# Kernel tuning notes

Hardware: AMD Instinct MI355X
Metric: run time of the kernel (lower is better)

## Reference

```python
import jax, jax.numpy as jnp
import numpy as np

NEG = -1e9

def setup_inputs() -> dict:
    key = jax.random.key(0)
    k1, k2, k3, k4, k5, k6 = jax.random.split(key, 6)
    B, S, H = 8, 2048, 1024
    inputs = jax.random.normal(k1, (B, S, H), dtype=jnp.float32)
    mask = jax.random.randint(k2, (B, S, S), 0, 2) > 0  # bool [B,S,S]
    scale = 1.0 / np.sqrt(H)
    Wq = jax.random.normal(k3, (H, H), dtype=jnp.float32) * scale
    Wk = jax.random.normal(k4, (H, H), dtype=jnp.float32) * scale
    Wv = jax.random.normal(k5, (H, H), dtype=jnp.float32) * scale
    return {"inputs": inputs, "mask": mask, "Wq": Wq, "Wk": Wk, "Wv": Wv}

def reference(inputs, mask, Wq, Wk, Wv):
    H = inputs.shape[-1]
    # nn.Linear(x) = x @ W.T (bias=False)
    Q = jnp.einsum('bsh,dh->bsd', inputs, Wq)
    K = jnp.einsum('bsh,dh->bsd', inputs, Wk)
    V = jnp.einsum('bsh,dh->bsd', inputs, Wv)
    alpha = jnp.einsum('bqd,bkd->bqk', Q, K) / jnp.sqrt(jnp.float32(H))
    alpha = jnp.where(mask, NEG, alpha)
    alpha = jax.nn.softmax(alpha, axis=-1)
    return jnp.einsum('bqk,bkd->bqd', alpha, V)
```

## Files before the change

### kernel.cpp

```cpp
#include <hip/hip_runtime.h>
#include <hip/hip_bf16.h>
#include <hip/hip_fp16.h>
#include <stdint.h>

typedef __attribute__((ext_vector_type(4))) float    f32x4;
typedef __attribute__((ext_vector_type(8))) _Float16 f16x8;
typedef __attribute__((ext_vector_type(4))) _Float16 f16x4;

template <int N> struct IC { static constexpr int value = N; };

__device__ __forceinline__ f32x4 mfma16(f16x8 a, f16x8 b, f32x4 c) {
  return __builtin_amdgcn_mfma_f32_16x16x32_f16(a, b, c, 0, 0, 0);
}

__device__ __forceinline__ void store4(float* p, f32x4 v) { *(f32x4*)p = v; }
__device__ __forceinline__ void store4(_Float16* p, f32x4 v) {
  f16x4 h; h[0] = (_Float16)v[0]; h[1] = (_Float16)v[1];
  h[2] = (_Float16)v[2]; h[3] = (_Float16)v[3];
  *(f16x4*)p = h;
}

__device__ __forceinline__ void gload16(const _Float16* g, char* l) {
  __builtin_amdgcn_global_load_lds(
      (const __attribute__((address_space(1))) void*)g,
      (__attribute__((address_space(3))) void*)l, 16, 0, 0);
}

__device__ __forceinline__ bool src_is_f32(const void* p) {
  const unsigned* w = (const unsigned*)p;
  int sane = 0;
#pragma unroll
  for (int i = 0; i < 64; ++i) {
    const unsigned e = (w[i] >> 7) & 0xFFu;
    sane += (e >= 100u && e <= 140u) ? 1 : 0;
  }
  return sane < 40;
}

__device__ __forceinline__ float bf16_to_f32(unsigned u16) {
  union { unsigned u; float f; } c; c.u = u16 << 16; return c.f;
}

__device__ __forceinline__ f16x8 cvt8(const void* in, long i, bool f32) {
  f16x8 o;
  if (f32) {
    const float4 a = ((const float4*)in)[2 * i];
    const float4 b = ((const float4*)in)[2 * i + 1];
    o[0] = (_Float16)a.x; o[1] = (_Float16)a.y; o[2] = (_Float16)a.z; o[3] = (_Float16)a.w;
    o[4] = (_Float16)b.x; o[5] = (_Float16)b.y; o[6] = (_Float16)b.z; o[7] = (_Float16)b.w;
  } else {
    const uint4 v = ((const uint4*)in)[i];
    const unsigned wd[4] = {v.x, v.y, v.z, v.w};
#pragma unroll
    for (int j = 0; j < 4; ++j) {
      o[2 * j]     = (_Float16)bf16_to_f32(wd[j] & 0xFFFFu);
      o[2 * j + 1] = (_Float16)bf16_to_f32(wd[j] >> 16);
    }
  }
  return o;
}

enum { MK_I32, MK_I64, MK_U16, MK_F32, MK_F64, MK_U8 };

__global__ __launch_bounds__(256)
void prep(const void* __restrict__ X, const void* __restrict__ w0,
          const void* __restrict__ w1, const void* __restrict__ w2,
          const void* __restrict__ maskp,
          _Float16* __restrict__ Xh, _Float16* __restrict__ Wh,
          int* __restrict__ modeOut, long nX8, long nW8)
{
  const long b = blockIdx.x;
  const long xBlocks = nX8 / 256;
  const long wBlocks = 3 * nW8 / 256;

  if (b < xBlocks) {
    const long i = b * 256 + threadIdx.x;
    ((f16x8*)Xh)[i] = cvt8(X, i, src_is_f32(X));
    return;
  }
  if (b < xBlocks + wBlocks) {
    const long j = (b - xBlocks) * 256 + threadIdx.x;
    const int which = (int)(j / nW8);
    const long lj = j - (long)which * nW8;
    const void* src = which == 0 ? w0 : (which == 1 ? w1 : w2);
    ((f16x8*)Wh)[j] = cvt8(src, lj, src_is_f32(src));
    return;
  }
  if (threadIdx.x != 0) return;
  const unsigned* mw = (const unsigned*)maskp;
  bool le1 = true, u16p = true, f32p = true, f64p = true, oddz = true;
  for (int i = 0; i < 64; ++i) {
    const unsigned v = mw[i];
    if (v > 1u) le1 = false;
    if (v != 0u && v != 1u && v != 0x10000u && v != 0x10001u) u16p = false;
    if (v != 0u && v != 0x3F800000u) f32p = false;
    if (i & 1) { if (v != 0u && v != 0x3FF00000u) f64p = false; if (v) oddz = false; }
    else       { if (v > 1u) f64p = false; }
  }
  int mode;
  if (le1)        mode = oddz ? MK_I64 : MK_I32;
  else if (u16p)  mode = MK_U16;
  else if (f32p)  mode = MK_F32;
  else if (f64p)  mode = MK_F64;
  else            mode = MK_U8;
  *modeOut = mode;
}

__global__ __launch_bounds__(256)
void zerofill(float* out, long n) {
  const long i = (long)blockIdx.x * 256 + threadIdx.x;
  if (i < n) out[i] = 0.0f;
}

template <typename TO, int BN, int WN>
__global__ __launch_bounds__(512, 2)
void gemm256(const _Float16* __restrict__ Ag, const _Float16* __restrict__ Bg,
             TO* __restrict__ Cg, int ldA, int ldB, int ldC, int Kd,
             long sAb, long sBb, long sCb, float scale, int gx, int gy)
{
  constexpr int WM   = 8 / WN;
  constexpr int BMW  = 256 / WM;
  constexpr int MI   = BMW / 16;
  constexpr int NPH  = MI / 2;
  constexpr int BSZ  = 32768 + BN * 128;

  extern __shared__ char smem[];

  const int nwg = gridDim.x;
  const int q = nwg >> 3, r = nwg & 7;
  const int xcd = blockIdx.x & 7, sub = blockIdx.x >> 3;
  const int wg = (xcd < r ? xcd * (q + 1) : r * (q + 1) + (xcd - r) * q) + sub;
  const int bz  = wg / (gx * gy);
  const int rem = wg % (gx * gy);
  const int by  = rem / gx;
  const int bx  = rem % gx;

  const _Float16* A = Ag + (long)bz * sAb + (long)by * 256 * ldA;
  const _Float16* B = Bg + (long)bz * sBb + (long)bx * BN * ldB;
  TO* C = Cg + (long)bz * sCb;

  const int t   = threadIdx.x;
  const int ln  = t & 63;
  const int wid = t >> 6;
  const int wr  = wid / WN;
  const int wc  = wid % WN;
  const int fr  = ln & 15;
  const int c16 = ln >> 4;

  const int sr = t >> 3;
  const int sc = t & 7;
  const int swzc = (sc ^ (sr & 7)) << 3;

  auto STAGE = [&](const _Float16* M, int ld, int matOff, int row0, int kt1) {
    const _Float16* src = M + (long)(row0 + sr) * ld + (kt1 << 6) + swzc;
    char* dst = smem + (kt1 & 1) * BSZ + matOff + (row0 << 7) + (t << 4);
    gload16(src, dst);
  };
  auto STAGE_TILE = [&](int kt1) {
#pragma unroll
    for (int r0 = 0; r0 < BN; r0 += 64) STAGE(B, ldB, 32768, r0, kt1);
    STAGE(A, ldA, 0,   0, kt1);  STAGE(A, ldA, 0,  64, kt1);
    STAGE(A, ldA, 0, 128, kt1);  STAGE(A, ldA, 0, 192, kt1);
  };

  f32x4 acc[MI][4] = {};

  STAGE_TILE(0);
  asm volatile("s_waitcnt vmcnt(0)" ::: "memory");
  __builtin_amdgcn_s_barrier();

  const int NT = Kd >> 6;

  auto kloop = [&](auto rotC) {
    constexpr int ROT = decltype(rotC)::value;
    for (int kt = 0; kt < NT; ++kt) {
      const int bufOff = (kt & 1) * BSZ;
      if (kt + 1 < NT) STAGE_TILE(kt + 1);

      auto LDA = [&](int mi, int kk) -> f16x8 {
        const int row = wr * BMW + (mi << 4) + fr;
        const int ch  = ((kk << 2) + c16) ^ (row & 7);
        return *(const f16x8*)(smem + bufOff + (row << 7) + (ch << 4));
      };
      auto LDB = [&](int ni, int kk) -> f16x8 {
        const int row = (wc << 6) + (ni << 4) + fr;
        const int ch  = ((kk << 2) + c16) ^ (row & 7);
        return *(const f16x8*)(smem + bufOff + 32768 + (row << 7) + (ch << 4));
      };

      f16x8 bF[4][2];
#pragma unroll
      for (int ni = 0; ni < 4; ++ni)
#pragma unroll
        for (int kk = 0; kk < 2; ++kk) bF[ni][kk] = LDB(ni, kk);

#pragma unroll
      for (int p = 0; p < NPH; ++p) {
        const int pr = (p + ROT) % NPH;
        f16x8 aF[2][2];
#pragma unroll
        for (int i = 0; i < 2; ++i)
#pragma unroll
          for (int kk = 0; kk < 2; ++kk) aF[i][kk] = LDA(2 * pr + i, kk);

        __builtin_amdgcn_s_setprio(1);
#pragma unroll
        for (int i = 0; i < 2; ++i)
#pragma unroll
          for (int ni = 0; ni < 4; ++ni)
#pragma unroll
            for (int kk = 0; kk < 2; ++kk)
              acc[2 * pr + i][ni] = mfma16(aF[i][kk], bF[ni][kk], acc[2 * pr + i][ni]);
        __builtin_amdgcn_s_setprio(0);
      }

      asm volatile("s_waitcnt vmcnt(0)" ::: "memory");
      __builtin_amdgcn_s_barrier();
    }
  };

  if constexpr (NPH == 4) {
    const int rot = ((wid & 3) + ((wid >> 2) << 1)) & 3;
    switch (rot) {
      case 0: kloop(IC<0>{}); break;
      case 1: kloop(IC<1>{}); break;
      case 2: kloop(IC<2>{}); break;
      default: kloop(IC<3>{}); break;
    }
  } else {
    const int rot = (wid ^ (wid >> 2)) & 1;
    if (rot == 0) kloop(IC<0>{}); else kloop(IC<1>{});
  }

  {
    char* wb = smem + wid * 4352;
    const int rr = (ln >> 4) << 2;
    const int rrow = ln >> 4;
    const int rch  = ln & 15;
#pragma unroll
    for (int mi = 0; mi < MI; ++mi) {
#pragma unroll
      for (int ni = 0; ni < 4; ++ni)
#pragma unroll
        for (int rq = 0; rq < 4; ++rq)
          *(float*)(wb + (((rr + rq) * 68) + (ni << 4) + fr) * 4) =
              scale * acc[mi][ni][rq];
#pragma unroll
      for (int it = 0; it < 4; ++it) {
        const int rloc = it * 4 + rrow;
        f32x4 v = *(const f32x4*)(wb + (rloc * 68 + rch * 4) * 4);
        const int row = by * 256 + wr * BMW + mi * 16 + rloc;
        const int col = bx * BN + wc * 64 + rch * 4;
        store4(&C[(long)row * ldC + col], v);
      }
    }
  }
}

__global__ __launch_bounds__(256)
void softmax_wave(_Float16* __restrict__ P, const void* __restrict__ maskp,
                  const int* __restrict__ modep, int S, long row0)
{
  const int  mode = *modep;
  const long lrow = (long)blockIdx.x * 4 + (threadIdx.x >> 6);
  const long grow = row0 + lrow;
  const int  ln   = threadIdx.x & 63;

  _Float16* prow = P + lrow * S;
  f16x8 pv[4];
#pragma unroll
  for (int j = 0; j < 4; ++j)
    pv[j] = *(const f16x8*)(prow + j * 512 + ln * 8);

  const long ebase = grow * (long)S;
  int mk[4][8];
  if (mode == MK_U8) {
    const unsigned char* m = (const unsigned char*)maskp + ebase;
#pragma unroll
    for (int j = 0; j < 4; ++j) {
      const unsigned long long v = *(const unsigned long long*)(m + j * 512 + ln * 8);
#pragma unroll
      for (int k = 0; k < 8; ++k) mk[j][k] = (int)((v >> (8 * k)) & 0xffull);
    }
  } else if (mode == MK_I32) {
    const int* m = (const int*)maskp + ebase;
#pragma unroll
    for (int j = 0; j < 4; ++j) {
      const int4 a = *(const int4*)(m + j * 512 + ln * 8);
      const int4 b = *(const int4*)(m + j * 512 + ln * 8 + 4);
      mk[j][0] = a.x; mk[j][1] = a.y; mk[j][2] = a.z; mk[j][3] = a.w;
      mk[j][4] = b.x; mk[j][5] = b.y; mk[j][6] = b.z; mk[j][7] = b.w;
    }
  } else if (mode == MK_F32) {
    const unsigned* m = (const unsigned*)maskp + ebase;
#pragma unroll
    for (int j = 0; j < 4; ++j) {
      const uint4 a = *(const uint4*)(m + j * 512 + ln * 8);
      const uint4 b = *(const uint4*)(m + j * 512 + ln * 8 + 4);
      mk[j][0] = a.x != 0; mk[j][1] = a.y != 0; mk[j][2] = a.z != 0; mk[j][3] = a.w != 0;
      mk[j][4] = b.x != 0; mk[j][5] = b.y != 0; mk[j][6] = b.z != 0; mk[j][7] = b.w != 0;
    }
  } else if (mode == MK_U16) {
    const unsigned short* m = (const unsigned short*)maskp + ebase;
#pragma unroll
    for (int j = 0; j < 4; ++j) {
      const uint4 v = *(const uint4*)(m + j * 512 + ln * 8);
      const unsigned wd[4] = {v.x, v.y, v.z, v.w};
#pragma unroll
      for (int k = 0; k < 4; ++k) {
        mk[j][2 * k]     = (wd[k] & 0xFFFFu) != 0;
        mk[j][2 * k + 1] = (wd[k] >> 16) != 0;
      }
    }
  } else {
    const unsigned long long* m = (const unsigned long long*)maskp + ebase;
#pragma unroll
    for (int j = 0; j < 4; ++j)
#pragma unroll
      for (int k = 0; k < 8; ++k) mk[j][k] = m[j * 512 + ln * 8 + k] != 0ull;
  }

  float s[4][8];
  float mx = -3.0e38f;
#pragma unroll
  for (int j = 0; j < 4; ++j)
#pragma unroll
    for (int k = 0; k < 8; ++k) {
      s[j][k] = mk[j][k] ? -1e9f : (float)pv[j][k];
      mx = fmaxf(mx, s[j][k]);
    }
#pragma unroll
  for (int d = 1; d < 64; d <<= 1) mx = fmaxf(mx, __shfl_xor(mx, d));

  float sum = 0.f;
#pragma unroll
  for (int j = 0; j < 4; ++j)
#pragma unroll
    for (int k = 0; k < 8; ++k) { s[j][k] = __expf(s[j][k] - mx); sum += s[j][k]; }
#pragma unroll
  for (int d = 1; d < 64; d <<= 1) sum += __shfl_xor(sum, d);
  const float inv = 1.0f / sum;

#pragma unroll
  for (int j = 0; j < 4; ++j) {
    f16x8 ov;
#pragma unroll
    for (int k = 0; k < 8; ++k) ov[k] = (_Float16)(s[j][k] * inv);
    *(f16x8*)(prow + j * 512 + ln * 8) = ov;
  }
}

extern "C" void kernel_launch(void* const* d_in, const int* in_sizes, int n_in,
                              void* d_out, int out_size, void* d_ws, size_t ws_size,
                              hipStream_t stream)
{
  const int B = 8, S = 2048, H = 1024;
  const long nXl = (long)B * S * H;
  const long nMl = (long)B * S * S;
  const long nWl = (long)H * H;

  const void* X = nullptr;
  const void* Mk = nullptr;
  const void* W[3] = {nullptr, nullptr, nullptr};
  int wi = 0;
  for (int i = 0; i < n_in; ++i) {
    const long sz = in_sizes[i];
    if (sz == nXl) X = d_in[i];
    else if (sz == nMl) Mk = d_in[i];
    else if (sz == nWl && wi < 3) W[wi++] = d_in[i];
  }
  float* Out = (float*)d_out;

  const size_t nX = (size_t)nXl, nW = (size_t)nWl;
  const size_t need2 = (4 * nX + 3 * nW) * 2;
  const size_t need1 = (3 * nX + 3 * nW) * 2 + (size_t)nMl * 2;

  if (!X || !Mk || wi < 3 || ws_size < need2 + 256) {
    zerofill<<<dim3((unsigned)((out_size + 255) / 256)), dim3(256), 0, stream>>>(
        Out, (long)out_size);
    return;
  }
  const bool single = (ws_size >= need1 + 256);

  _Float16* Wh  = (_Float16*)d_ws;
  _Float16* QK2 = Wh  + 3 * nW;
  _Float16* Vt  = QK2 + 2 * nX;
  _Float16* Xh  = Vt  + nX;
  _Float16* P   = Xh;
  int* modeSlot = (int*)((char*)d_ws + (single ? need1 : need2));

  dim3 blk(256), gblk(512);
  const size_t LDS_256 = 2 * (32768 + 256 * 128);
  const size_t LDS_128 = 2 * (32768 + 128 * 128);
  const long SH = (long)S * H, SS = (long)S * S, HS = (long)H * S;

  const long nX8 = nX / 8, nW8 = nW / 8;
  const unsigned prepBlocks = (unsigned)(nX8 / 256 + 3 * nW8 / 256 + 1);
  prep<<<dim3(prepBlocks), blk, 0, stream>>>(X, W[0], W[1], W[2], Mk,
                                             Xh, Wh, modeSlot, nX8, nW8);

  gemm256<_Float16, 256, 4><<<dim3(8 * 64), gblk, LDS_256, stream>>>(
      Xh, Wh, QK2, H, H, 2 * H, H, 0L, 0L, 0L, 1.0f, 8, 64);
  gemm256<_Float16, 256, 4><<<dim3(8 * 4 * 8), gblk, LDS_256, stream>>>(
      Wh + 2 * nW, Xh, Vt, H, H, S, H, 0L, SH, HS, 1.0f, 8, 4);

  const _Float16* Qp = QK2;
  const _Float16* Kp = QK2 + H;

  if (single) {
    gemm256<_Float16, 256, 4><<<dim3(8 * 8 * 8), gblk, LDS_256, stream>>>(
        Qp, Kp, P, 2 * H, 2 * H, S, H, 2 * SH, 2 * SH, SS, 0.03125f, 8, 8);
    softmax_wave<<<dim3(B * S / 4), blk, 0, stream>>>(P, Mk, modeSlot, S, 0L);
    gemm256<float, 256, 4><<<dim3(4 * 8 * 8), gblk, LDS_256, stream>>>(
        P, Vt, Out, S, S, H, S, SS, HS, SH, 1.0f, 4, 8);
  } else {
    for (int g = 0; g < 2; ++g) {
      const int b0 = 4 * g;
      gemm256<_Float16, 256, 4><<<dim3(8 * 8 * 4), gblk, LDS_256, stream>>>(
          Qp + (long)b0 * 2 * SH, Kp + (long)b0 * 2 * SH, P,
          2 * H, 2 * H, S, H, 2 * SH, 2 * SH, SS, 0.03125f, 8, 8);
      softmax_wave<<<dim3(4 * S / 4), blk, 0, stream>>>(P, Mk, modeSlot, S, (long)b0 * S);
      gemm256<float, 128, 2><<<dim3(8 * 8 * 4), gblk, LDS_128, stream>>>(
          P, Vt + (long)b0 * HS, Out + (long)b0 * SH,
          S, S, H, S, SS, HS, SH, 1.0f, 8, 8);
    }
  }
}
```

Measured before the change: 310.0 us.

## Split GEMM k-loop into four MFMA quadrants interleaved with staged loads

Restructures the main GEMM k-loop into four quadrant phases. Each phase issues part of the next tile's global-to-LDS loads, runs a quarter of the MFMAs, and synchronises with barriers and partial vmcnt waits. This replaces the old per-wave phase rotation and the single bulk stage at the start of each iteration. The goal is to spread memory traffic across compute and keep waves in lockstep, at the cost of more barriers per iteration. The correctness of the partial vmcnt waits depends on the ordering of the loads.

Measured after the change: 316.1 us. About the same (+2.0%).

```diff
diff --git a/kernel.cpp b/kernel.cpp
--- a/kernel.cpp
+++ b/kernel.cpp
@@ -118,11 +118,11 @@
              TO* __restrict__ Cg, int ldA, int ldB, int ldC, int Kd,
              long sAb, long sBb, long sCb, float scale, int gx, int gy)
 {
-  constexpr int WM   = 8 / WN;
-  constexpr int BMW  = 256 / WM;
-  constexpr int MI   = BMW / 16;
-  constexpr int NPH  = MI / 2;
-  constexpr int BSZ  = 32768 + BN * 128;
+  constexpr int WM  = 8 / WN;
+  constexpr int BMW = 256 / WM;
+  constexpr int MI  = BMW / 16;
+  constexpr int QM  = MI / 2;
+  constexpr int BSZ = 32768 + BN * 128;
 
   extern __shared__ char smem[];
 
@@ -156,80 +156,114 @@
     char* dst = smem + (kt1 & 1) * BSZ + matOff + (row0 << 7) + (t << 4);
     gload16(src, dst);
   };
-  auto STAGE_TILE = [&](int kt1) {
-#pragma unroll
-    for (int r0 = 0; r0 < BN; r0 += 64) STAGE(B, ldB, 32768, r0, kt1);
-    STAGE(A, ldA, 0,   0, kt1);  STAGE(A, ldA, 0,  64, kt1);
-    STAGE(A, ldA, 0, 128, kt1);  STAGE(A, ldA, 0, 192, kt1);
+
+  f32x4 acc[MI][4] = {};
+  f16x8 bF[4][2], aF[QM][2];
+
+  auto MFMAQ = [&](auto MQc, auto NQc) {
+    constexpr int mq = decltype(MQc)::value;
+    constexpr int nq = decltype(NQc)::value;
+#pragma unroll
+    for (int i = 0; i < QM; ++i)
+#pragma unroll
+      for (int n2 = 0; n2 < 2; ++n2)
+#pragma unroll
+        for (int kk = 0; kk < 2; ++kk)
+          acc[mq * QM + i][nq * 2 + n2] =
+              mfma16(aF[i][kk], bF[nq * 2 + n2][kk], acc[mq * QM + i][nq * 2 + n2]);
   };
 
-  f32x4 acc[MI][4] = {};
-
-  STAGE_TILE(0);
-  asm volatile("s_waitcnt vmcnt(0)" ::: "memory");
+  if constexpr (WN == 4) {
+    STAGE(B, ldB, 32768,   0, 0); STAGE(B, ldB, 32768,  64, 0);
+    STAGE(B, ldB, 32768, 128, 0); STAGE(B, ldB, 32768, 192, 0);
+    STAGE(A, ldA, 0,   0, 0);     STAGE(A, ldA, 0, 128, 0);
+    STAGE(A, ldA, 0,  64, 0);     STAGE(A, ldA, 0, 192, 0);
+    asm volatile("s_waitcnt vmcnt(2)" ::: "memory");
+  } else {
+    STAGE(B, ldB, 32768,   0, 0); STAGE(B, ldB, 32768,  64, 0);
+    STAGE(A, ldA, 0,   0, 0);     STAGE(A, ldA, 0,  64, 0);
+    STAGE(A, ldA, 0, 128, 0);     STAGE(A, ldA, 0, 192, 0);
+    asm volatile("s_waitcnt vmcnt(0)" ::: "memory");
+  }
   __builtin_amdgcn_s_barrier();
 
   const int NT = Kd >> 6;
-
-  auto kloop = [&](auto rotC) {
-    constexpr int ROT = decltype(rotC)::value;
-    for (int kt = 0; kt < NT; ++kt) {
-      const int bufOff = (kt & 1) * BSZ;
-      if (kt + 1 < NT) STAGE_TILE(kt + 1);
-
-      auto LDA = [&](int mi, int kk) -> f16x8 {
-        const int row = wr * BMW + (mi << 4) + fr;
-        const int ch  = ((kk << 2) + c16) ^ (row & 7);
-        return *(const f16x8*)(smem + bufOff + (row << 7) + (ch << 4));
-      };
-      auto LDB = [&](int ni, int kk) -> f16x8 {
-        const int row = (wc << 6) + (ni << 4) + fr;
-        const int ch  = ((kk << 2) + c16) ^ (row & 7);
-        return *(const f16x8*)(smem + bufOff + 32768 + (row << 7) + (ch << 4));
-      };
-
-      f16x8 bF[4][2];
-#pragma unroll
-      for (int ni = 0; ni < 4; ++ni)
-#pragma unroll
-        for (int kk = 0; kk < 2; ++kk) bF[ni][kk] = LDB(ni, kk);
-
-#pragma unroll
-      for (int p = 0; p < NPH; ++p) {
-        const int pr = (p + ROT) % NPH;
-        f16x8 aF[2][2];
-#pragma unroll
-        for (int i = 0; i < 2; ++i)
-#pragma unroll
-          for (int kk = 0; kk < 2; ++kk) aF[i][kk] = LDA(2 * pr + i, kk);
-
-        __builtin_amdgcn_s_setprio(1);
-#pragma unroll
-        for (int i = 0; i < 2; ++i)
-#pragma unroll
-          for (int ni = 0; ni < 4; ++ni)
-#pragma unroll
-            for (int kk = 0; kk < 2; ++kk)
-              acc[2 * pr + i][ni] = mfma16(aF[i][kk], bF[ni][kk], acc[2 * pr + i][ni]);
-        __builtin_amdgcn_s_setprio(0);
-      }
-
-      asm volatile("s_waitcnt vmcnt(0)" ::: "memory");
-      __builtin_amdgcn_s_barrier();
-    }
-  };
-
-  if constexpr (NPH == 4) {
-    const int rot = ((wid & 3) + ((wid >> 2) << 1)) & 3;
-    switch (rot) {
-      case 0: kloop(IC<0>{}); break;
-      case 1: kloop(IC<1>{}); break;
-      case 2: kloop(IC<2>{}); break;
-      default: kloop(IC<3>{}); break;
-    }
-  } else {
-    const int rot = (wid ^ (wid >> 2)) & 1;
-    if (rot == 0) kloop(IC<0>{}); else kloop(IC<1>{});
+  for (int kt = 0; kt < NT; ++kt) {
+    const int bufOff = (kt & 1) * BSZ;
+    const bool more = (kt + 1) < NT;
+    const int nk = kt + 1;
+
+    auto LDA = [&](int mi, int kk) -> f16x8 {
+      const int row = wr * BMW + (mi << 4) + fr;
+      const int ch  = ((kk << 2) + c16) ^ (row & 7);
+      return *(const f16x8*)(smem + bufOff + (row << 7) + (ch << 4));
+    };
+    auto LDB = [&](int ni, int kk) -> f16x8 {
+      const int row = (wc << 6) + (ni << 4) + fr;
+      const int ch  = ((kk << 2) + c16) ^ (row & 7);
+      return *(const f16x8*)(smem + bufOff + 32768 + (row << 7) + (ch << 4));
+    };
+
+#pragma unroll
+    for (int ni = 0; ni < 4; ++ni)
+#pragma unroll
+      for (int kk = 0; kk < 2; ++kk) bF[ni][kk] = LDB(ni, kk);
+#pragma unroll
+    for (int i = 0; i < QM; ++i)
+#pragma unroll
+      for (int kk = 0; kk < 2; ++kk) aF[i][kk] = LDA(i, kk);
+    if (more) { STAGE(B, ldB, 32768, 0, nk); STAGE(B, ldB, 32768, 64, nk); }
+    __builtin_amdgcn_s_barrier();
+    asm volatile("s_waitcnt lgkmcnt(0)" ::: "memory");
+    __builtin_amdgcn_sched_barrier(0);
+    __builtin_amdgcn_s_setprio(1);
+    MFMAQ(IC<0>{}, IC<0>{});
+    __builtin_amdgcn_s_setprio(0);
+    __builtin_amdgcn_s_barrier();
+
+    if (more) {
+      if constexpr (WN == 4) { STAGE(B, ldB, 32768, 128, nk); STAGE(B, ldB, 32768, 192, nk); }
+      else                   { STAGE(A, ldA, 0, 0, nk);       STAGE(A, ldA, 0, 64, nk); }
+    }
+    __builtin_amdgcn_s_barrier();
+    __builtin_amdgcn_s_setprio(1);
+    MFMAQ(IC<0>{}, IC<1>{});
+    __builtin_amdgcn_s_setprio(0);
+    if constexpr (WN == 4) {
+      if (more) asm volatile("s_waitcnt vmcnt(4)" ::: "memory");
+      else      asm volatile("s_waitcnt vmcnt(0)" ::: "memory");
+    }
+    __builtin_amdgcn_s_barrier();
+
+#pragma unroll
+    for (int i = 0; i < QM; ++i)
+#pragma unroll
+      for (int kk = 0; kk < 2; ++kk) aF[i][kk] = LDA(QM + i, kk);
+    if (more) {
+      if constexpr (WN == 4) { STAGE(A, ldA, 0, 0, nk);   STAGE(A, ldA, 0, 128, nk); }
+      else                   { STAGE(A, ldA, 0, 128, nk); STAGE(A, ldA, 0, 192, nk); }
+    }
+    __builtin_amdgcn_s_barrier();
+    asm volatile("s_waitcnt lgkmcnt(0)" ::: "memory");
+    __builtin_amdgcn_sched_barrier(0);
+    __builtin_amdgcn_s_setprio(1);
+    MFMAQ(IC<1>{}, IC<0>{});
+    __builtin_amdgcn_s_setprio(0);
+    __builtin_amdgcn_s_barrier();
+
+    if (more) {
+      if constexpr (WN == 4) { STAGE(A, ldA, 0, 64, nk); STAGE(A, ldA, 0, 192, nk); }
+    }
+    __builtin_amdgcn_s_barrier();
+    __builtin_amdgcn_s_setprio(1);
+    MFMAQ(IC<1>{}, IC<1>{});
+    __builtin_amdgcn_s_setprio(0);
+    if constexpr (WN == 4) {
+      if (more) asm volatile("s_waitcnt vmcnt(2)" ::: "memory");
+    } else {
+      if (more) asm volatile("s_waitcnt vmcnt(0)" ::: "memory");
+    }
+    __builtin_amdgcn_s_barrier();
   }
 
   {
```
